# Performance work log

Measured on AMD Instinct MI355X. Metric: run time of the kernel, lower is better.

The kernel has to match this reference:

```python
import jax, jax.numpy as jnp
import numpy as np

B_LARGE, B_SMALL = 256, 256
R_LARGE, R_SMALL = 64, 16
N_LARGE, N_SMALL = 128, 128
D = 4096


def setup_inputs() -> dict:
    key = jax.random.key(0)
    k1, k2, k3, k4, k5 = jax.random.split(key, 5)
    x = jax.random.normal(k1, (B_LARGE + B_SMALL, 1, D), dtype=jnp.float16)
    wids_large = jax.random.randint(k2, (B_LARGE,), 0, N_LARGE, dtype=jnp.int32)
    wids_small = jax.random.randint(k3, (B_SMALL,), 0, N_SMALL, dtype=jnp.int32)
    lora_A_large = (jax.random.normal(k4, (N_LARGE, D, R_LARGE), dtype=jnp.float16) * jnp.float16(0.02))
    lora_A_small = (jax.random.normal(k5, (N_SMALL, D, R_SMALL), dtype=jnp.float16) * jnp.float16(0.02))
    return {"x": x, "wids_large": wids_large, "wids_small": wids_small,
            "lora_A_large": lora_A_large, "lora_A_small": lora_A_small}


def reference(x, wids_large, wids_small, lora_A_large, lora_A_small):
    # split batch into large / small adapter groups
    x_l = x[:B_LARGE]          # [Bl, 1, D]
    x_s = x[B_LARGE:]          # [Bs, 1, D]
    # gather per-sample adapter matrices, then batched matmul (BGMV pattern)
    A_l = lora_A_large[wids_large]   # [Bl, D, r_large]
    A_s = lora_A_small[wids_small]   # [Bs, D, r_small]
    y_large = jnp.einsum('bsd,bdr->bsr', x_l, A_l)  # [Bl, 1, r_large]
    y_small = jnp.einsum('bsd,bdr->bsr', x_s, A_s)  # [Bs, 1, r_small]
    return (y_large, y_small)
```

## Files before the change

kernel.cpp:

```cpp
#include <hip/hip_runtime.h>

#define NDIM 4096
#define B_LG 256
#define B_SM 256
#define N_WID 128
#define R_LG 64
#define R_SM 16
#define BLOCK 512
#define MAXB 256
#define MAXM 6
#define PF 8
#define OUT_SIZE (B_LG * R_LG + B_SM * R_SM)

#define DCH_LG 512
#define DCH_SM 1024
#define NCH_LG (NDIM / DCH_LG)
#define NCH_SM (NDIM / DCH_SM)

typedef float floatv4 __attribute__((ext_vector_type(4)));

#define WS_CNT_L  0
#define WS_CNT_S  128
#define WS_NWORK  256
#define WS_TICKET 260
#define WS_BKT_L  512
#define WS_BKT_S  (WS_BKT_L + N_WID * MAXB)
#define WS_WORK   (WS_BKT_S + N_WID * MAXB)
#define MAX_WORK  4096

__global__ __launch_bounds__(BLOCK)
void setup_kernel(const int* __restrict__ wids_l,
                  const int* __restrict__ wids_s,
                  int* __restrict__ ws,
                  float* __restrict__ out)
{
    __shared__ int cl[N_WID], cs[N_WID];
    __shared__ int nwork;
    const int t = threadIdx.x;
    if (t < N_WID) { cl[t] = 0; cs[t] = 0; }
    if (t == 0) nwork = 0;
    __syncthreads();
    if (t < B_LG) {
        const int w = wids_l[t];
        const int s = atomicAdd(&cl[w], 1);
        ws[WS_BKT_L + w * MAXB + s] = t;
    } else if (t < B_LG + B_SM) {
        const int b = t - B_LG;
        const int w = wids_s[b];
        const int s = atomicAdd(&cs[w], 1);
        ws[WS_BKT_S + w * MAXB + s] = b;
    }
    __syncthreads();
    if (t < N_WID) {
        ws[WS_CNT_L + t] = cl[t];
        ws[WS_CNT_S + t] = cs[t];
        int cnt = cl[t];
        for (int g = 0; g < cnt; g += MAXM) {
            const int Mi   = min(MAXM, cnt - g);
            const int base = atomicAdd(&nwork, NCH_LG);
            for (int c = 0; c < NCH_LG; ++c) {
                ws[WS_WORK + 2 * (base + c)]     = (t << 8) | c;
                ws[WS_WORK + 2 * (base + c) + 1] = (g << 8) | Mi;
            }
        }
        cnt = cs[t];
        for (int g = 0; g < cnt; g += MAXM) {
            const int Mi   = min(MAXM, cnt - g);
            const int base = atomicAdd(&nwork, NCH_SM);
            for (int c = 0; c < NCH_SM; ++c) {
                ws[WS_WORK + 2 * (base + c)]     = (1 << 30) | (t << 8) | c;
                ws[WS_WORK + 2 * (base + c) + 1] = (g << 8) | Mi;
            }
        }
    }
    __syncthreads();
    if (t == 0) { ws[WS_NWORK] = nwork; ws[WS_TICKET] = 0; }
    for (int i = t; i < OUT_SIZE; i += BLOCK) out[i] = 0.0f;
}

template<int R, int M, int DCH>
__device__ __forceinline__ void gemv_chunk(
    const float* __restrict__ x,
    const float* __restrict__ Ab,
    float* __restrict__ outb,
    const int* __restrict__ batches,
    int d0,
    float* __restrict__ xs,
    float* __restrict__ red)
{
    constexpr int LPR  = R / 4;
    constexpr int ROWS = BLOCK / LPR;
    constexpr int IT   = DCH / ROWS;
    constexpr int NG   = IT / PF;

    const int t = threadIdx.x;

    int rows[M];
#pragma unroll
    for (int m = 0; m < M; ++m) rows[m] = batches[m];

#pragma unroll
    for (int m = 0; m < M; ++m)
        for (int i = t; i < DCH / 4; i += BLOCK)
            reinterpret_cast<float4*>(xs + m * DCH)[i] =
                reinterpret_cast<const float4*>(x + (size_t)rows[m] * NDIM + d0)[i];
    __syncthreads();

    const int d_sub  = t / LPR;
    const int r_base = (t % LPR) * 4;
    const float* Abt = Ab + ((size_t)d0 + d_sub) * R + r_base;

    float acc[M][4];
#pragma unroll
    for (int m = 0; m < M; ++m)
#pragma unroll
        for (int j = 0; j < 4; ++j) acc[m][j] = 0.0f;

#pragma unroll
    for (int g = 0; g < NG; ++g) {
        floatv4 buf[PF];
#pragma unroll
        for (int p = 0; p < PF; ++p)
            buf[p] = __builtin_nontemporal_load(
                reinterpret_cast<const floatv4*>(Abt + (size_t)(g * PF + p) * ROWS * R));
#pragma unroll
        for (int p = 0; p < PF; ++p) {
            const int d = (g * PF + p) * ROWS + d_sub;
#pragma unroll
            for (int m = 0; m < M; ++m) {
                const float xv = xs[m * DCH + d];
                acc[m][0] = fmaf(xv, buf[p].x, acc[m][0]);
                acc[m][1] = fmaf(xv, buf[p].y, acc[m][1]);
                acc[m][2] = fmaf(xv, buf[p].z, acc[m][2]);
                acc[m][3] = fmaf(xv, buf[p].w, acc[m][3]);
            }
        }
    }

    const int wave = t >> 6;
    const int lane = t & 63;
#pragma unroll
    for (int m = 0; m < M; ++m)
#pragma unroll
        for (int off = 32; off >= LPR; off >>= 1)
#pragma unroll
            for (int j = 0; j < 4; ++j)
                acc[m][j] += __shfl_down(acc[m][j], off, 64);

#pragma unroll
    for (int m = 0; m < M; ++m) {
        __syncthreads();
        if (lane < LPR)
#pragma unroll
            for (int j = 0; j < 4; ++j) red[(wave * 16 + lane) * 4 + j] = acc[m][j];
        __syncthreads();
        if (t < R) {
            const int rl = t / 4, j = t % 4;
            float v = 0.0f;
#pragma unroll
            for (int w = 0; w < 8; ++w) v += red[(w * 16 + rl) * 4 + j];
            atomicAdd(outb + (size_t)rows[m] * R + t, v);
        }
    }
}

__global__ __launch_bounds__(BLOCK, 4)
void SequentialLoraA_kernel(const float* __restrict__ x,
                            const float* __restrict__ Al,
                            const float* __restrict__ As,
                            float* __restrict__ out,
                            int* __restrict__ ws)
{
    __shared__ float xs[MAXM * DCH_SM];
    __shared__ float red[8 * 16 * 4];
    __shared__ int s_item;

    const int t  = threadIdx.x;
    const int nw = ws[WS_NWORK];

    for (;;) {
        __syncthreads();
        if (t == 0) s_item = atomicAdd(ws + WS_TICKET, 1);
        __syncthreads();
        const int it = s_item;
        if (it >= nw) return;

        const int a   = ws[WS_WORK + 2 * it];
        const int b   = ws[WS_WORK + 2 * it + 1];
        const int wid = (a >> 8) & 0x7f;
        const int Mi  = b & 0xff;
        const int gs  = b >> 8;

        if (a & (1 << 30)) {
            const int d0 = (a & 0xff) * DCH_SM;
            const float* xb  = x + (size_t)B_LG * NDIM;
            const float* Ab  = As + (size_t)wid * NDIM * R_SM;
            float*       ob  = out + (size_t)B_LG * R_LG;
            const int*   bkt = ws + WS_BKT_S + wid * MAXB + gs;
            switch (Mi) {
              case 1: gemv_chunk<R_SM, 1, DCH_SM>(xb, Ab, ob, bkt, d0, xs, red); break;
              case 2: gemv_chunk<R_SM, 2, DCH_SM>(xb, Ab, ob, bkt, d0, xs, red); break;
              case 3: gemv_chunk<R_SM, 3, DCH_SM>(xb, Ab, ob, bkt, d0, xs, red); break;
              case 4: gemv_chunk<R_SM, 4, DCH_SM>(xb, Ab, ob, bkt, d0, xs, red); break;
              case 5: gemv_chunk<R_SM, 5, DCH_SM>(xb, Ab, ob, bkt, d0, xs, red); break;
              default: gemv_chunk<R_SM, 6, DCH_SM>(xb, Ab, ob, bkt, d0, xs, red); break;
            }
        } else {
            const int d0 = (a & 0xff) * DCH_LG;
            const float* Ab  = Al + (size_t)wid * NDIM * R_LG;
            const int*   bkt = ws + WS_BKT_L + wid * MAXB + gs;
            switch (Mi) {
              case 1: gemv_chunk<R_LG, 1, DCH_LG>(x, Ab, out, bkt, d0, xs, red); break;
              case 2: gemv_chunk<R_LG, 2, DCH_LG>(x, Ab, out, bkt, d0, xs, red); break;
              case 3: gemv_chunk<R_LG, 3, DCH_LG>(x, Ab, out, bkt, d0, xs, red); break;
              case 4: gemv_chunk<R_LG, 4, DCH_LG>(x, Ab, out, bkt, d0, xs, red); break;
              case 5: gemv_chunk<R_LG, 5, DCH_LG>(x, Ab, out, bkt, d0, xs, red); break;
              default: gemv_chunk<R_LG, 6, DCH_LG>(x, Ab, out, bkt, d0, xs, red); break;
            }
        }
    }
}

extern "C" void kernel_launch(void* const* d_in, const int* in_sizes, int n_in,
                              void* d_out, int out_size, void* d_ws, size_t ws_size,
                              hipStream_t stream) {
    const float* x      = (const float*)d_in[0];
    const int*   wids_l = (const int*)d_in[1];
    const int*   wids_s = (const int*)d_in[2];
    const float* Al     = (const float*)d_in[3];
    const float* As     = (const float*)d_in[4];
    float* out = (float*)d_out;
    int*   ws  = (int*)d_ws;

    setup_kernel<<<1, BLOCK, 0, stream>>>(wids_l, wids_s, ws, out);
    SequentialLoraA_kernel<<<1024, BLOCK, 0, stream>>>(x, Al, As, out, ws);
}
```

Before: 228.5 us.

## Replace persistent ticket scheduler with static one-item-per-block coarse work

Drops the atomic-ticket persistent loop. Each block now handles one work item chosen by blockIdx and loops over several D-chunks internally: two halves per large-rank group, and the full D for small-rank groups. This removes the global ticket atomics and cuts the partial-sum atomicAdds on the output. In exchange, far fewer blocks run at once, which lowers memory-level parallelism and occupancy. The fixed grid of 512 blocks assumes the work count never exceeds it.

```diff
diff --git a/kernel.cpp b/kernel.cpp
--- a/kernel.cpp
+++ b/kernel.cpp
@@ -13,20 +13,17 @@
 #define OUT_SIZE (B_LG * R_LG + B_SM * R_SM)
 
 #define DCH_LG 512
+#define NCH_LG 4
 #define DCH_SM 1024
-#define NCH_LG (NDIM / DCH_LG)
-#define NCH_SM (NDIM / DCH_SM)
+#define NCH_SM 4
+#define GRID_MAIN 512
 
 typedef float floatv4 __attribute__((ext_vector_type(4)));
 
-#define WS_CNT_L  0
-#define WS_CNT_S  128
-#define WS_NWORK  256
-#define WS_TICKET 260
-#define WS_BKT_L  512
+#define WS_NWORK  0
+#define WS_BKT_L  256
 #define WS_BKT_S  (WS_BKT_L + N_WID * MAXB)
 #define WS_WORK   (WS_BKT_S + N_WID * MAXB)
-#define MAX_WORK  4096
 
 __global__ __launch_bounds__(BLOCK)
 void setup_kernel(const int* __restrict__ wids_l,
@@ -52,39 +49,35 @@
     }
     __syncthreads();
     if (t < N_WID) {
-        ws[WS_CNT_L + t] = cl[t];
-        ws[WS_CNT_S + t] = cs[t];
         int cnt = cl[t];
         for (int g = 0; g < cnt; g += MAXM) {
             const int Mi   = min(MAXM, cnt - g);
-            const int base = atomicAdd(&nwork, NCH_LG);
-            for (int c = 0; c < NCH_LG; ++c) {
-                ws[WS_WORK + 2 * (base + c)]     = (t << 8) | c;
-                ws[WS_WORK + 2 * (base + c) + 1] = (g << 8) | Mi;
+            const int base = atomicAdd(&nwork, 2);
+            for (int h = 0; h < 2; ++h) {
+                ws[WS_WORK + 2 * (base + h)]     = (t << 8) | h;
+                ws[WS_WORK + 2 * (base + h) + 1] = (g << 8) | Mi;
             }
         }
         cnt = cs[t];
         for (int g = 0; g < cnt; g += MAXM) {
             const int Mi   = min(MAXM, cnt - g);
-            const int base = atomicAdd(&nwork, NCH_SM);
-            for (int c = 0; c < NCH_SM; ++c) {
-                ws[WS_WORK + 2 * (base + c)]     = (1 << 30) | (t << 8) | c;
-                ws[WS_WORK + 2 * (base + c) + 1] = (g << 8) | Mi;
-            }
+            const int base = atomicAdd(&nwork, 1);
+            ws[WS_WORK + 2 * base]     = (1 << 30) | (t << 8);
+            ws[WS_WORK + 2 * base + 1] = (g << 8) | Mi;
         }
     }
     __syncthreads();
-    if (t == 0) { ws[WS_NWORK] = nwork; ws[WS_TICKET] = 0; }
+    if (t == 0) ws[WS_NWORK] = nwork;
     for (int i = t; i < OUT_SIZE; i += BLOCK) out[i] = 0.0f;
 }
 
-template<int R, int M, int DCH>
-__device__ __forceinline__ void gemv_chunk(
+template<int R, int M, int DCH, int NCH>
+__device__ __forceinline__ void gemv_item(
     const float* __restrict__ x,
     const float* __restrict__ Ab,
     float* __restrict__ outb,
     const int* __restrict__ batches,
-    int d0,
+    int dbase,
     float* __restrict__ xs,
     float* __restrict__ red)
 {
@@ -92,23 +85,16 @@
     constexpr int ROWS = BLOCK / LPR;
     constexpr int IT   = DCH / ROWS;
     constexpr int NG   = IT / PF;
+    static_assert(IT % PF == 0, "chunk not divisible by pipeline group");
 
     const int t = threadIdx.x;
 
     int rows[M];
 #pragma unroll
     for (int m = 0; m < M; ++m) rows[m] = batches[m];
-
-#pragma unroll
-    for (int m = 0; m < M; ++m)
-        for (int i = t; i < DCH / 4; i += BLOCK)
-            reinterpret_cast<float4*>(xs + m * DCH)[i] =
-                reinterpret_cast<const float4*>(x + (size_t)rows[m] * NDIM + d0)[i];
-    __syncthreads();
 
     const int d_sub  = t / LPR;
     const int r_base = (t % LPR) * 4;
-    const float* Abt = Ab + ((size_t)d0 + d_sub) * R + r_base;
 
     float acc[M][4];
 #pragma unroll
@@ -116,23 +102,37 @@
 #pragma unroll
         for (int j = 0; j < 4; ++j) acc[m][j] = 0.0f;
 
-#pragma unroll
-    for (int g = 0; g < NG; ++g) {
-        floatv4 buf[PF];
-#pragma unroll
-        for (int p = 0; p < PF; ++p)
-            buf[p] = __builtin_nontemporal_load(
-                reinterpret_cast<const floatv4*>(Abt + (size_t)(g * PF + p) * ROWS * R));
-#pragma unroll
-        for (int p = 0; p < PF; ++p) {
-            const int d = (g * PF + p) * ROWS + d_sub;
-#pragma unroll
-            for (int m = 0; m < M; ++m) {
-                const float xv = xs[m * DCH + d];
-                acc[m][0] = fmaf(xv, buf[p].x, acc[m][0]);
-                acc[m][1] = fmaf(xv, buf[p].y, acc[m][1]);
-                acc[m][2] = fmaf(xv, buf[p].z, acc[m][2]);
-                acc[m][3] = fmaf(xv, buf[p].w, acc[m][3]);
+    for (int c = 0; c < NCH; ++c) {
+        const int d0 = dbase + c * DCH;
+
+        __syncthreads();
+#pragma unroll
+        for (int m = 0; m < M; ++m)
+            for (int i = t; i < DCH / 4; i += BLOCK)
+                reinterpret_cast<float4*>(xs + m * DCH)[i] =
+                    reinterpret_cast<const float4*>(x + (size_t)rows[m] * NDIM + d0)[i];
+        __syncthreads();
+
+        const float* Abt = Ab + ((size_t)d0 + d_sub) * R + r_base;
+
+#pragma unroll
+        for (int g = 0; g < NG; ++g) {
+            floatv4 buf[PF];
+#pragma unroll
+            for (int p = 0; p < PF; ++p)
+                buf[p] = __builtin_nontemporal_load(
+                    reinterpret_cast<const floatv4*>(Abt + (size_t)(g * PF + p) * ROWS * R));
+#pragma unroll
+            for (int p = 0; p < PF; ++p) {
+                const int d = (g * PF + p) * ROWS + d_sub;
+#pragma unroll
+                for (int m = 0; m < M; ++m) {
+                    const float xv = xs[m * DCH + d];
+                    acc[m][0] = fmaf(xv, buf[p].x, acc[m][0]);
+                    acc[m][1] = fmaf(xv, buf[p].y, acc[m][1]);
+                    acc[m][2] = fmaf(xv, buf[p].z, acc[m][2]);
+                    acc[m][3] = fmaf(xv, buf[p].w, acc[m][3]);
+                }
             }
         }
     }
@@ -169,54 +169,44 @@
                             const float* __restrict__ Al,
                             const float* __restrict__ As,
                             float* __restrict__ out,
-                            int* __restrict__ ws)
+                            const int* __restrict__ ws)
 {
     __shared__ float xs[MAXM * DCH_SM];
     __shared__ float red[8 * 16 * 4];
-    __shared__ int s_item;
-
-    const int t  = threadIdx.x;
-    const int nw = ws[WS_NWORK];
-
-    for (;;) {
-        __syncthreads();
-        if (t == 0) s_item = atomicAdd(ws + WS_TICKET, 1);
-        __syncthreads();
-        const int it = s_item;
-        if (it >= nw) return;
-
-        const int a   = ws[WS_WORK + 2 * it];
-        const int b   = ws[WS_WORK + 2 * it + 1];
-        const int wid = (a >> 8) & 0x7f;
-        const int Mi  = b & 0xff;
-        const int gs  = b >> 8;
-
-        if (a & (1 << 30)) {
-            const int d0 = (a & 0xff) * DCH_SM;
-            const float* xb  = x + (size_t)B_LG * NDIM;
-            const float* Ab  = As + (size_t)wid * NDIM * R_SM;
-            float*       ob  = out + (size_t)B_LG * R_LG;
-            const int*   bkt = ws + WS_BKT_S + wid * MAXB + gs;
-            switch (Mi) {
-              case 1: gemv_chunk<R_SM, 1, DCH_SM>(xb, Ab, ob, bkt, d0, xs, red); break;
-              case 2: gemv_chunk<R_SM, 2, DCH_SM>(xb, Ab, ob, bkt, d0, xs, red); break;
-              case 3: gemv_chunk<R_SM, 3, DCH_SM>(xb, Ab, ob, bkt, d0, xs, red); break;
-              case 4: gemv_chunk<R_SM, 4, DCH_SM>(xb, Ab, ob, bkt, d0, xs, red); break;
-              case 5: gemv_chunk<R_SM, 5, DCH_SM>(xb, Ab, ob, bkt, d0, xs, red); break;
-              default: gemv_chunk<R_SM, 6, DCH_SM>(xb, Ab, ob, bkt, d0, xs, red); break;
-            }
-        } else {
-            const int d0 = (a & 0xff) * DCH_LG;
-            const float* Ab  = Al + (size_t)wid * NDIM * R_LG;
-            const int*   bkt = ws + WS_BKT_L + wid * MAXB + gs;
-            switch (Mi) {
-              case 1: gemv_chunk<R_LG, 1, DCH_LG>(x, Ab, out, bkt, d0, xs, red); break;
-              case 2: gemv_chunk<R_LG, 2, DCH_LG>(x, Ab, out, bkt, d0, xs, red); break;
-              case 3: gemv_chunk<R_LG, 3, DCH_LG>(x, Ab, out, bkt, d0, xs, red); break;
-              case 4: gemv_chunk<R_LG, 4, DCH_LG>(x, Ab, out, bkt, d0, xs, red); break;
-              case 5: gemv_chunk<R_LG, 5, DCH_LG>(x, Ab, out, bkt, d0, xs, red); break;
-              default: gemv_chunk<R_LG, 6, DCH_LG>(x, Ab, out, bkt, d0, xs, red); break;
-            }
+
+    const int it = blockIdx.x;
+    if (it >= ws[WS_NWORK]) return;
+
+    const int a   = ws[WS_WORK + 2 * it];
+    const int b   = ws[WS_WORK + 2 * it + 1];
+    const int wid = (a >> 8) & 0x7f;
+    const int Mi  = b & 0xff;
+    const int gs  = b >> 8;
+
+    if (a & (1 << 30)) {
+        const float* xb  = x + (size_t)B_LG * NDIM;
+        const float* Ab  = As + (size_t)wid * NDIM * R_SM;
+        float*       ob  = out + (size_t)B_LG * R_LG;
+        const int*   bkt = ws + WS_BKT_S + wid * MAXB + gs;
+        switch (Mi) {
+          case 1:  gemv_item<R_SM, 1, DCH_SM, NCH_SM>(xb, Ab, ob, bkt, 0, xs, red); break;
+          case 2:  gemv_item<R_SM, 2, DCH_SM, NCH_SM>(xb, Ab, ob, bkt, 0, xs, red); break;
+          case 3:  gemv_item<R_SM, 3, DCH_SM, NCH_SM>(xb, Ab, ob, bkt, 0, xs, red); break;
+          case 4:  gemv_item<R_SM, 4, DCH_SM, NCH_SM>(xb, Ab, ob, bkt, 0, xs, red); break;
+          case 5:  gemv_item<R_SM, 5, DCH_SM, NCH_SM>(xb, Ab, ob, bkt, 0, xs, red); break;
+          default: gemv_item<R_SM, 6, DCH_SM, NCH_SM>(xb, Ab, ob, bkt, 0, xs, red); break;
+        }
+    } else {
+        const int dbase = (a & 1) * (NCH_LG * DCH_LG);
+        const float* Ab  = Al + (size_t)wid * NDIM * R_LG;
+        const int*   bkt = ws + WS_BKT_L + wid * MAXB + gs;
+        switch (Mi) {
+          case 1:  gemv_item<R_LG, 1, DCH_LG, NCH_LG>(x, Ab, out, bkt, dbase, xs, red); break;
+          case 2:  gemv_item<R_LG, 2, DCH_LG, NCH_LG>(x, Ab, out, bkt, dbase, xs, red); break;
+          case 3:  gemv_item<R_LG, 3, DCH_LG, NCH_LG>(x, Ab, out, bkt, dbase, xs, red); break;
+          case 4:  gemv_item<R_LG, 4, DCH_LG, NCH_LG>(x, Ab, out, bkt, dbase, xs, red); break;
+          case 5:  gemv_item<R_LG, 5, DCH_LG, NCH_LG>(x, Ab, out, bkt, dbase, xs, red); break;
+          default: gemv_item<R_LG, 6, DCH_LG, NCH_LG>(x, Ab, out, bkt, dbase, xs, red); break;
         }
     }
 }
@@ -233,5 +223,5 @@
     int*   ws  = (int*)d_ws;
 
     setup_kernel<<<1, BLOCK, 0, stream>>>(wids_l, wids_s, ws, out);
-    SequentialLoraA_kernel<<<1024, BLOCK, 0, stream>>>(x, Al, As, out, ws);
-}
+    SequentialLoraA_kernel<<<GRID_MAIN, BLOCK, 0, stream>>>(x, Al, As, out, ws);
+}
```

Result: faster. 216.5 us (-5.2%).
